# Kernel tuning notes

Hardware: AMD Instinct MI355X
Metric: run time of the kernel (lower is better)

The kernel has to match this reference:

```python
import jax, jax.numpy as jnp
import numpy as np

FP8_MAX = 448.0  # torch.finfo(float8_e4m3fn).max
TINY = float(np.finfo(np.float32).tiny)
BN = BK = 128  # block sizes


def _make_fp8_weight(key, N, K):
    """Mirror _create_fp8_weight: per-128x128-block scales, fp8 quantized values."""
    w = jax.random.normal(key, (N, K), jnp.float32) * 0.01
    wb = w.reshape(N // BN, BN, K // BK, BK)
    amax = jnp.abs(wb).max(axis=(1, 3))
    scale_inv = jnp.maximum(amax / FP8_MAX, TINY)  # [N/BN, K/BK]
    wq = (wb / scale_inv[:, None, :, None]).reshape(N, K)
    wq = wq.astype(jnp.float8_e4m3fn).astype(jnp.float32)  # fp8-rounded values
    return wq, scale_inv


def _dequant(wq, scale_inv):
    N, K = wq.shape
    nb, kb = scale_inv.shape
    wb = wq.reshape(nb, N // nb, kb, K // kb) * scale_inv[:, None, :, None]
    return wb.reshape(N, K)


def setup_inputs() -> dict:
    key = jax.random.key(0)
    kx, k1, k2, k3 = jax.random.split(key, 4)
    T, H, F = 4096, 2048, 7168  # tokens, hidden_dim, ffn_dim
    x = jax.random.normal(kx, (T, H), jnp.float32)
    w1_q, w1_s = _make_fp8_weight(k1, F, H)
    w3_q, w3_s = _make_fp8_weight(k3, F, H)
    w2_q, w2_s = _make_fp8_weight(k2, H, F)
    return {"hidden_states": x, "w1_q": w1_q, "w1_s": w1_s,
            "w3_q": w3_q, "w3_s": w3_s, "w2_q": w2_q, "w2_s": w2_s}


def reference(hidden_states, w1_q, w1_s, w3_q, w3_s, w2_q, w2_s):
    x = hidden_states
    w1 = _dequant(w1_q, w1_s)  # [F, H]
    w3 = _dequant(w3_q, w3_s)  # [F, H]
    w2 = _dequant(w2_q, w2_s)  # [H, F]
    g = x @ w1.T               # [T, F]
    u = x @ w3.T               # [T, F]
    fused = jax.nn.silu(g) * u
    return fused @ w2.T        # [T, H]
```

## Files before the change

kernel.cpp:

```cpp
#include <hip/hip_runtime.h>
#include <stdint.h>

typedef __attribute__((ext_vector_type(8))) short short8;
typedef __attribute__((ext_vector_type(4))) float floatx4;

__device__ __forceinline__ unsigned short f2bf(float f) {
  union { float f; unsigned int u; } c; c.f = f;
  unsigned int u = c.u;
  unsigned int r = (u + 0x7fffu + ((u >> 16) & 1u)) >> 16;
  return (unsigned short)r;
}
__device__ __forceinline__ float bf2f(unsigned short h) {
  union { unsigned int u; float f; } c; c.u = ((unsigned int)h) << 16;
  return c.f;
}

__device__ __forceinline__ void load16_to_lds(const void* g, void* l) {
  __builtin_amdgcn_global_load_lds(
      (const __attribute__((address_space(1))) unsigned int*)g,
      (__attribute__((address_space(3))) unsigned int*)l, 16, 0, 0);
}

__global__ void f32_to_bf16_kernel(const float* __restrict__ in,
                                   unsigned short* __restrict__ out, long n4) {
  long i = blockIdx.x * (long)blockDim.x + threadIdx.x;
  if (i >= n4) return;
  float4 v = ((const float4*)in)[i];
  ushort4 o;
  o.x = f2bf(v.x); o.y = f2bf(v.y); o.z = f2bf(v.z); o.w = f2bf(v.w);
  ((ushort4*)out)[i] = o;
}

__global__ void dequant2_kernel(const float* __restrict__ w1q,
                                const float* __restrict__ s1,
                                const float* __restrict__ w3q,
                                const float* __restrict__ s3,
                                unsigned short* __restrict__ o1,
                                unsigned short* __restrict__ o3,
                                int K, int sK) {
  int n = blockIdx.y;
  int k = blockIdx.x * 1024 + threadIdx.x * 4;
  size_t idx = (size_t)n * K + k;
  int sidx = (n >> 7) * sK + (k >> 7);
  float sc1 = s1[sidx], sc3 = s3[sidx];
  float4 v1 = *(const float4*)(w1q + idx);
  float4 v3 = *(const float4*)(w3q + idx);
  ushort4 a, b;
  a.x = f2bf(v1.x * sc1); a.y = f2bf(v1.y * sc1);
  a.z = f2bf(v1.z * sc1); a.w = f2bf(v1.w * sc1);
  b.x = f2bf(v3.x * sc3); b.y = f2bf(v3.y * sc3);
  b.z = f2bf(v3.z * sc3); b.w = f2bf(v3.w * sc3);
  *(ushort4*)(o1 + idx) = a;
  *(ushort4*)(o3 + idx) = b;
}

__global__ void dequant1_kernel(const float* __restrict__ wq,
                                const float* __restrict__ s,
                                unsigned short* __restrict__ out,
                                int K, int sK) {
  int n = blockIdx.y;
  int k = blockIdx.x * 1024 + threadIdx.x * 4;
  size_t idx = (size_t)n * K + k;
  float sc = s[(n >> 7) * sK + (k >> 7)];
  float4 v = *(const float4*)(wq + idx);
  ushort4 o;
  o.x = f2bf(v.x * sc); o.y = f2bf(v.y * sc);
  o.z = f2bf(v.z * sc); o.w = f2bf(v.w * sc);
  *(ushort4*)(out + idx) = o;
}


__global__ __launch_bounds__(512, 4) void dual_gemm_silu(
    const unsigned short* __restrict__ A,
    const unsigned short* __restrict__ B1,
    const unsigned short* __restrict__ B3,
    unsigned short* __restrict__ C,
    int M, int N, int K) {
  __shared__ unsigned short As[128 * 64];
  __shared__ unsigned short B1s[128 * 64];
  __shared__ unsigned short B3s[128 * 64];

  const int tid = threadIdx.x;
  const int lane = tid & 63;
  const int wave = tid >> 6;
  const int wm = wave >> 2;
  const int wn = wave & 3;
  const int m0 = blockIdx.y * 128, n0 = blockIdx.x * 128;

  const int s0 = tid, s1 = tid + 512;
  const int r0 = s0 >> 3, c0 = ((s0 & 7) ^ (r0 & 7)) * 8;
  const int r1 = s1 >> 3, c1 = ((s1 & 7) ^ (r1 & 7)) * 8;

  const int q = lane >> 4;
  const int r16 = lane & 15;
  const int rx = r16 & 7;

  floatx4 acc_g[4][2], acc_u[4][2];
#pragma unroll
  for (int i = 0; i < 4; i++)
#pragma unroll
    for (int j = 0; j < 2; j++) {
      acc_g[i][j] = (floatx4){0.f, 0.f, 0.f, 0.f};
      acc_u[i][j] = (floatx4){0.f, 0.f, 0.f, 0.f};
    }

  const unsigned short* ag0 = A + (size_t)(m0 + r0) * K + c0;
  const unsigned short* ag1 = A + (size_t)(m0 + r1) * K + c1;
  const unsigned short* b1g0 = B1 + (size_t)(n0 + r0) * K + c0;
  const unsigned short* b1g1 = B1 + (size_t)(n0 + r1) * K + c1;
  const unsigned short* b3g0 = B3 + (size_t)(n0 + r0) * K + c0;
  const unsigned short* b3g1 = B3 + (size_t)(n0 + r1) * K + c1;

  for (int k0 = 0; k0 < K; k0 += 64) {
    load16_to_lds(ag0 + k0, &As[s0 * 8]);
    load16_to_lds(ag1 + k0, &As[s1 * 8]);
    load16_to_lds(b1g0 + k0, &B1s[s0 * 8]);
    load16_to_lds(b1g1 + k0, &B1s[s1 * 8]);
    load16_to_lds(b3g0 + k0, &B3s[s0 * 8]);
    load16_to_lds(b3g1 + k0, &B3s[s1 * 8]);
    __syncthreads();

#pragma unroll
    for (int kh = 0; kh < 2; kh++) {
      const int kq = kh * 4 + q;
      short8 a[4], b1v[2], b3v[2];
#pragma unroll
      for (int t = 0; t < 4; t++) {
        int row = wm * 64 + t * 16 + r16;
        a[t] = *(const short8*)&As[(row * 8 + (kq ^ rx)) * 8];
      }
#pragma unroll
      for (int j = 0; j < 2; j++) {
        int row = wn * 32 + j * 16 + r16;
        int u = (row * 8 + (kq ^ rx)) * 8;
        b1v[j] = *(const short8*)&B1s[u];
        b3v[j] = *(const short8*)&B3s[u];
      }
#pragma unroll
      for (int i = 0; i < 4; i++)
#pragma unroll
        for (int j = 0; j < 2; j++) {
          acc_g[i][j] = __builtin_amdgcn_mfma_f32_16x16x32_bf16(
              a[i], b1v[j], acc_g[i][j], 0, 0, 0);
          acc_u[i][j] = __builtin_amdgcn_mfma_f32_16x16x32_bf16(
              a[i], b3v[j], acc_u[i][j], 0, 0, 0);
        }
    }
    __syncthreads();
  }

#pragma unroll
  for (int i = 0; i < 4; i++) {
    int row0 = m0 + wm * 64 + i * 16 + q * 4;
#pragma unroll
    for (int j = 0; j < 2; j++) {
      int col = n0 + wn * 32 + j * 16 + r16;
#pragma unroll
      for (int rr = 0; rr < 4; rr++) {
        float gv = acc_g[i][j][rr];
        float uv = acc_u[i][j][rr];
        float sv = gv / (1.f + __expf(-gv)) * uv;
        C[(size_t)(row0 + rr) * N + col] = f2bf(sv);
      }
    }
  }
}

__global__ __launch_bounds__(256, 4) void gemm_nt_f32_n64(
    const unsigned short* __restrict__ A,
    const unsigned short* __restrict__ B,
    float* __restrict__ C,
    int M, int N, int K) {
  __shared__ unsigned short As[128 * 64];
  __shared__ unsigned short Bs[64 * 64];

  const int tid = threadIdx.x;
  const int lane = tid & 63;
  const int wave = tid >> 6;
  const int wm = wave >> 1;
  const int wn = wave & 1;
  const int m0 = blockIdx.y * 128, n0 = blockIdx.x * 64;

  const int q = lane >> 4;
  const int r16 = lane & 15;
  const int rx = r16 & 7;

  floatx4 acc[4][2];
#pragma unroll
  for (int i = 0; i < 4; i++)
#pragma unroll
    for (int j = 0; j < 2; j++) acc[i][j] = (floatx4){0.f, 0.f, 0.f, 0.f};

  int aoff[4], adst[4];
#pragma unroll
  for (int p = 0; p < 4; p++) {
    int u = tid + 256 * p;
    int r = u >> 3;
    int c = ((u & 7) ^ (r & 7)) * 8;
    aoff[p] = r * K + c;
    adst[p] = u * 8;
  }
  int boff[2], bdst[2];
#pragma unroll
  for (int p = 0; p < 2; p++) {
    int u = tid + 256 * p;
    int r = u >> 3;
    int c = ((u & 7) ^ (r & 7)) * 8;
    boff[p] = r * K + c;
    bdst[p] = u * 8;
  }

  const unsigned short* Abase = A + (size_t)m0 * K;
  const unsigned short* Bbase = B + (size_t)n0 * K;

  for (int k0 = 0; k0 < K; k0 += 64) {
#pragma unroll
    for (int p = 0; p < 4; p++)
      load16_to_lds(Abase + aoff[p] + k0, &As[adst[p]]);
#pragma unroll
    for (int p = 0; p < 2; p++)
      load16_to_lds(Bbase + boff[p] + k0, &Bs[bdst[p]]);
    __syncthreads();

#pragma unroll
    for (int kh = 0; kh < 2; kh++) {
      const int kq = kh * 4 + q;
      short8 a[4], b[2];
#pragma unroll
      for (int t = 0; t < 4; t++) {
        int row = wm * 64 + t * 16 + r16;
        a[t] = *(const short8*)&As[(row * 8 + (kq ^ rx)) * 8];
      }
#pragma unroll
      for (int j = 0; j < 2; j++) {
        int row = wn * 32 + j * 16 + r16;
        b[j] = *(const short8*)&Bs[(row * 8 + (kq ^ rx)) * 8];
      }
#pragma unroll
      for (int i = 0; i < 4; i++)
#pragma unroll
        for (int j = 0; j < 2; j++)
          acc[i][j] = __builtin_amdgcn_mfma_f32_16x16x32_bf16(
              a[i], b[j], acc[i][j], 0, 0, 0);
    }
    __syncthreads();
  }

#pragma unroll
  for (int i = 0; i < 4; i++) {
    int row0 = m0 + wm * 64 + i * 16 + q * 4;
#pragma unroll
    for (int j = 0; j < 2; j++) {
      int col = n0 + wn * 32 + j * 16 + r16;
#pragma unroll
      for (int rr = 0; rr < 4; rr++)
        C[(size_t)(row0 + rr) * N + col] = acc[i][j][rr];
    }
  }
}

extern "C" void kernel_launch(void* const* d_in, const int* in_sizes, int n_in,
                              void* d_out, int out_size, void* d_ws, size_t ws_size,
                              hipStream_t stream) {
  const float* x = (const float*)d_in[0];
  const float* w1q = (const float*)d_in[1];
  const float* w1s = (const float*)d_in[2];
  const float* w3q = (const float*)d_in[3];
  const float* w3s = (const float*)d_in[4];
  const float* w2q = (const float*)d_in[5];
  const float* w2s = (const float*)d_in[6];

  const int T = 4096, H = 2048, F = 7168;

  char* ws = (char*)d_ws;
  unsigned short* xb  = (unsigned short*)ws;  ws += (size_t)T * H * 2;
  unsigned short* w1b = (unsigned short*)ws;  ws += (size_t)F * H * 2;
  unsigned short* w3b = (unsigned short*)ws;  ws += (size_t)F * H * 2;
  unsigned short* w2b = (unsigned short*)ws;  ws += (size_t)H * F * 2;
  unsigned short* g   = (unsigned short*)ws;  ws += (size_t)T * F * 2;

  long xn4 = (long)T * H / 4;

  f32_to_bf16_kernel<<<(xn4 + 255) / 256, 256, 0, stream>>>(x, xb, xn4);
  dequant2_kernel<<<dim3(H / 1024, F), 256, 0, stream>>>(
      w1q, w1s, w3q, w3s, w1b, w3b, H, H / 128);
  dequant1_kernel<<<dim3(F / 1024, H), 256, 0, stream>>>(
      w2q, w2s, w2b, F, F / 128);

  dual_gemm_silu<<<dim3(F / 128, T / 128), 512, 0, stream>>>(xb, w1b, w3b, g, T, F, H);

  gemm_nt_f32_n64<<<dim3(H / 64, T / 128), 256, 0, stream>>>(g, w2b, (float*)d_out, T, H, F);
}
```

Measured before the change: 593.5 us.

## Use 128x128 tiles with split-K over two slices and atomic accumulation

The down-projection GEMM moves from 128x64 output tiles to 128x128 tiles, raising MFMA work per LDS load. To keep enough blocks in flight, K is split in half across a third grid dimension. Partial sums are combined with float atomic adds into an output zeroed by a memset beforehand. The price is the extra memset, atomic traffic on the output, fewer resident blocks per CU under the lower launch bound, and nondeterministic summation order.

```diff
diff --git a/kernel.cpp b/kernel.cpp
--- a/kernel.cpp
+++ b/kernel.cpp
@@ -166,80 +166,72 @@
   }
 }
 
-__global__ __launch_bounds__(256, 4) void gemm_nt_f32_n64(
+__global__ __launch_bounds__(256, 2) void gemm_nt_f32_sk(
     const unsigned short* __restrict__ A,
     const unsigned short* __restrict__ B,
     float* __restrict__ C,
     int M, int N, int K) {
   __shared__ unsigned short As[128 * 64];
-  __shared__ unsigned short Bs[64 * 64];
+  __shared__ unsigned short Bs[128 * 64];
 
   const int tid = threadIdx.x;
   const int lane = tid & 63;
   const int wave = tid >> 6;
   const int wm = wave >> 1;
   const int wn = wave & 1;
-  const int m0 = blockIdx.y * 128, n0 = blockIdx.x * 64;
-
-  const int q = lane >> 4;
-  const int r16 = lane & 15;
-  const int rx = r16 & 7;
-
-  floatx4 acc[4][2];
-#pragma unroll
-  for (int i = 0; i < 4; i++)
-#pragma unroll
-    for (int j = 0; j < 2; j++) acc[i][j] = (floatx4){0.f, 0.f, 0.f, 0.f};
-
-  int aoff[4], adst[4];
+  const int m0 = blockIdx.y * 128, n0 = blockIdx.x * 128;
+  const int kbase = blockIdx.z * (K >> 1);
+  const int kend = kbase + (K >> 1);
+
+  int soff[4], sdst[4];
 #pragma unroll
   for (int p = 0; p < 4; p++) {
     int u = tid + 256 * p;
     int r = u >> 3;
     int c = ((u & 7) ^ (r & 7)) * 8;
-    aoff[p] = r * K + c;
-    adst[p] = u * 8;
-  }
-  int boff[2], bdst[2];
-#pragma unroll
-  for (int p = 0; p < 2; p++) {
-    int u = tid + 256 * p;
-    int r = u >> 3;
-    int c = ((u & 7) ^ (r & 7)) * 8;
-    boff[p] = r * K + c;
-    bdst[p] = u * 8;
-  }
+    soff[p] = r * K + c;
+    sdst[p] = u * 8;
+  }
+
+  const int q = lane >> 4;
+  const int r16 = lane & 15;
+  const int rx = r16 & 7;
+
+  floatx4 acc[4][4];
+#pragma unroll
+  for (int i = 0; i < 4; i++)
+#pragma unroll
+    for (int j = 0; j < 4; j++) acc[i][j] = (floatx4){0.f, 0.f, 0.f, 0.f};
 
   const unsigned short* Abase = A + (size_t)m0 * K;
   const unsigned short* Bbase = B + (size_t)n0 * K;
 
-  for (int k0 = 0; k0 < K; k0 += 64) {
-#pragma unroll
-    for (int p = 0; p < 4; p++)
-      load16_to_lds(Abase + aoff[p] + k0, &As[adst[p]]);
-#pragma unroll
-    for (int p = 0; p < 2; p++)
-      load16_to_lds(Bbase + boff[p] + k0, &Bs[bdst[p]]);
+  for (int k0 = kbase; k0 < kend; k0 += 64) {
+#pragma unroll
+    for (int p = 0; p < 4; p++) {
+      load16_to_lds(Abase + soff[p] + k0, &As[sdst[p]]);
+      load16_to_lds(Bbase + soff[p] + k0, &Bs[sdst[p]]);
+    }
     __syncthreads();
 
 #pragma unroll
     for (int kh = 0; kh < 2; kh++) {
       const int kq = kh * 4 + q;
-      short8 a[4], b[2];
+      short8 a[4], b[4];
 #pragma unroll
       for (int t = 0; t < 4; t++) {
         int row = wm * 64 + t * 16 + r16;
         a[t] = *(const short8*)&As[(row * 8 + (kq ^ rx)) * 8];
       }
 #pragma unroll
-      for (int j = 0; j < 2; j++) {
-        int row = wn * 32 + j * 16 + r16;
+      for (int j = 0; j < 4; j++) {
+        int row = wn * 64 + j * 16 + r16;
         b[j] = *(const short8*)&Bs[(row * 8 + (kq ^ rx)) * 8];
       }
 #pragma unroll
       for (int i = 0; i < 4; i++)
 #pragma unroll
-        for (int j = 0; j < 2; j++)
+        for (int j = 0; j < 4; j++)
           acc[i][j] = __builtin_amdgcn_mfma_f32_16x16x32_bf16(
               a[i], b[j], acc[i][j], 0, 0, 0);
     }
@@ -250,11 +242,11 @@
   for (int i = 0; i < 4; i++) {
     int row0 = m0 + wm * 64 + i * 16 + q * 4;
 #pragma unroll
-    for (int j = 0; j < 2; j++) {
-      int col = n0 + wn * 32 + j * 16 + r16;
+    for (int j = 0; j < 4; j++) {
+      int col = n0 + wn * 64 + j * 16 + r16;
 #pragma unroll
       for (int rr = 0; rr < 4; rr++)
-        C[(size_t)(row0 + rr) * N + col] = acc[i][j][rr];
+        unsafeAtomicAdd(&C[(size_t)(row0 + rr) * N + col], acc[i][j][rr]);
     }
   }
 }
@@ -289,5 +281,7 @@
 
   dual_gemm_silu<<<dim3(F / 128, T / 128), 512, 0, stream>>>(xb, w1b, w3b, g, T, F, H);
 
-  gemm_nt_f32_n64<<<dim3(H / 64, T / 128), 256, 0, stream>>>(g, w2b, (float*)d_out, T, H, F);
-}
+  hipMemsetAsync(d_out, 0, (size_t)T * H * 4, stream);
+  gemm_nt_f32_sk<<<dim3(H / 128, T / 128, 2), 256, 0, stream>>>(
+      g, w2b, (float*)d_out, T, H, F);
+}
```

Result: no change. 582.9 us (-1.8%).
